# Optimization experiments

Hardware: AMD Instinct MI355X
Metric: run time of the kernel (lower is better)

## Reference

```python
import jax, jax.numpy as jnp
import numpy as np

POOL_SIZE = 7
NUM_ROIS = 1024
H, W, C = 256, 256, 512


def setup_inputs() -> dict:
    key = jax.random.key(0)
    k_img, k_xy, k_wh = jax.random.split(key, 3)
    img = jax.random.normal(k_img, (1, H, W, C), dtype=jnp.float32)
    # Valid ROIs: top-left in [0, 192), size in [8, 64), clipped to image bounds.
    xy = jax.random.randint(k_xy, (1, NUM_ROIS, 2), 0, 192)          # (x1, y1)
    wh = jax.random.randint(k_wh, (1, NUM_ROIS, 2), 8, 64)           # (w, h)
    x1y1 = xy
    x2y2 = jnp.minimum(xy + wh, jnp.array([W, H]))
    rois = jnp.concatenate([x1y1, x2y2], axis=-1).astype(jnp.int32)  # [1, R, 4] = (x1, y1, x2, y2)
    return {"img": img, "rois": rois}


def _roi_resize(feat, roi, P):
    """Bilinear-resize crop feat[y1:y2, x1:x2, :] to (P, P) — TF1 legacy mapping.
    feat: [H, W, C] float, roi: [4] int32 (x1, y1, x2, y2). Returns [P, P, C]."""
    x1, y1, x2, y2 = roi[0], roi[1], roi[2], roi[3]
    h = (y2 - y1).astype(jnp.float32)
    w = (x2 - x1).astype(jnp.float32)
    # src coordinate (crop-relative) = out_idx * (in_size / out_size)
    ys = jnp.arange(P, dtype=jnp.float32) * (h / P)   # [P]
    xs = jnp.arange(P, dtype=jnp.float32) * (w / P)   # [P]
    y0 = jnp.floor(ys).astype(jnp.int32)
    x0 = jnp.floor(xs).astype(jnp.int32)
    y1i = jnp.minimum(y0 + 1, jnp.maximum(y2 - y1 - 1, 0))
    x1i = jnp.minimum(x0 + 1, jnp.maximum(x2 - x1 - 1, 0))
    wy = (ys - y0.astype(jnp.float32))[:, None, None]  # [P,1,1]
    wx = (xs - x0.astype(jnp.float32))[None, :, None]  # [1,P,1]
    r0, r1 = y1 + y0, y1 + y1i                         # absolute rows
    c0, c1 = x1 + x0, x1 + x1i                         # absolute cols
    v00 = feat[r0[:, None], c0[None, :], :]            # [P,P,C]
    v01 = feat[r0[:, None], c1[None, :], :]
    v10 = feat[r1[:, None], c0[None, :], :]
    v11 = feat[r1[:, None], c1[None, :], :]
    return (v00 * (1.0 - wy) * (1.0 - wx) + v01 * (1.0 - wy) * wx
            + v10 * wy * (1.0 - wx) + v11 * wy * wx)


def reference(img, rois):
    feat = img[0]                                       # [H, W, C]
    pooled = jax.vmap(_roi_resize, in_axes=(None, 0, None))(feat, rois[0], POOL_SIZE)
    return pooled[None]                                 # [1, num_rois, P, P, C]
```

## Files before the change

### kernel.cpp

```cpp
#include <hip/hip_runtime.h>

#define POOL 7
#define IMG_W 256
#define IMG_C 512
#define NUM_ROIS 1024

typedef float f4 __attribute__((ext_vector_type(4)));

__global__ __launch_bounds__(128) void roi_pool_kernel(
    const float* __restrict__ img,
    const int*   __restrict__ rois,
    float*       __restrict__ out)
{
    const int bid  = blockIdx.x;
    const int xcd  = bid & 7;
    const int slot = bid >> 3;
    const int rloc = slot / POOL;
    const int py   = slot - rloc * POOL;
    const int roi  = xcd * (NUM_ROIS / 8) + rloc;

    const int4 rb = ((const int4*)rois)[roi];
    const int x1 = __builtin_amdgcn_readfirstlane(rb.x);
    const int y1 = __builtin_amdgcn_readfirstlane(rb.y);
    const int x2 = __builtin_amdgcn_readfirstlane(rb.z);
    const int y2 = __builtin_amdgcn_readfirstlane(rb.w);

    const float h = (float)(y2 - y1);
    const float w = (float)(x2 - x1);
    const float sy = h / (float)POOL;
    const float sx = w / (float)POOL;

    const float ys = (float)py * sy;
    const int   y0 = (int)floorf(ys);
    const int   y1i = min(y0 + 1, max(y2 - y1 - 1, 0));
    const float wy = ys - (float)y0;

    const size_t rowstride = (size_t)IMG_W * IMG_C;
    const float* row0 = img + (size_t)(y1 + y0)  * rowstride;
    const float* row1 = img + (size_t)(y1 + y1i) * rowstride;

    const int t = threadIdx.x;
    f4* obase = (f4*)out + ((size_t)roi * (POOL * POOL) + (size_t)py * POOL) * (IMG_C / 4) + t;

    const int cmax = max(x2 - x1 - 1, 0);

#pragma unroll
    for (int px = 0; px < POOL; ++px) {
        const float xs = (float)px * sx;
        const int   x0 = (int)floorf(xs);
        const int   x1i = min(x0 + 1, cmax);
        const float wx = xs - (float)x0;
        const int c0 = x1 + x0, c1 = x1 + x1i;

        const f4 v00 = ((const f4*)(row0 + (size_t)c0 * IMG_C))[t];
        const f4 v01 = ((const f4*)(row0 + (size_t)c1 * IMG_C))[t];
        const f4 v10 = ((const f4*)(row1 + (size_t)c0 * IMG_C))[t];
        const f4 v11 = ((const f4*)(row1 + (size_t)c1 * IMG_C))[t];

        const float w00 = (1.0f - wy) * (1.0f - wx);
        const float w01 = (1.0f - wy) * wx;
        const float w10 = wy * (1.0f - wx);
        const float w11 = wy * wx;

        f4 o = v00 * w00 + v01 * w01 + v10 * w10 + v11 * w11;
        __builtin_nontemporal_store(o, obase + px * (IMG_C / 4));
    }
}

extern "C" void kernel_launch(void* const* d_in, const int* in_sizes, int n_in,
                              void* d_out, int out_size, void* d_ws, size_t ws_size,
                              hipStream_t stream) {
    const float* img  = (const float*)d_in[0];
    const int*   rois = (const int*)d_in[1];
    float* out = (float*)d_out;

    dim3 grid(NUM_ROIS * POOL);
    dim3 block(128);
    roi_pool_kernel<<<grid, block, 0, stream>>>(img, rois, out);
}
```

Baseline: 236.5 us.

## Sort ROIs by spatial bin so blocks on an XCD share cached image rows

Adds a one-block counting-sort kernel that orders ROIs by a coarse 32x32-pixel spatial bucket of their top-left corner. The pooling kernel then processes ROIs in this sorted order, so ROIs handled by the same XCD are spatially close and reuse image data in that XCD's L2. The cost is an extra kernel launch, a dependent index load per block, and workspace use, and output writes become scattered across ROIs.

Result: no change. 234.9 us (-0.7%).

```diff
diff --git a/kernel.cpp b/kernel.cpp
--- a/kernel.cpp
+++ b/kernel.cpp
@@ -7,17 +7,45 @@
 
 typedef float f4 __attribute__((ext_vector_type(4)));
 
+__global__ __launch_bounds__(1024) void sort_rois_kernel(
+    const int* __restrict__ rois, int* __restrict__ order)
+{
+    __shared__ int hist[64];
+    __shared__ int base[64];
+    const int tid = threadIdx.x;
+
+    if (tid < 64) hist[tid] = 0;
+    __syncthreads();
+
+    const int x1 = rois[4 * tid + 0];
+    const int y1 = rois[4 * tid + 1];
+    const int key = ((y1 >> 5) << 3) | (x1 >> 5);
+    const int rank = atomicAdd(&hist[key], 1);
+    __syncthreads();
+
+    if (tid == 0) {
+        int run = 0;
+#pragma unroll
+        for (int k = 0; k < 64; ++k) { base[k] = run; run += hist[k]; }
+    }
+    __syncthreads();
+
+    order[base[key] + rank] = tid;
+}
+
 __global__ __launch_bounds__(128) void roi_pool_kernel(
     const float* __restrict__ img,
     const int*   __restrict__ rois,
+    const int*   __restrict__ order,
     float*       __restrict__ out)
 {
     const int bid  = blockIdx.x;
     const int xcd  = bid & 7;
     const int slot = bid >> 3;
-    const int rloc = slot / POOL;
-    const int py   = slot - rloc * POOL;
-    const int roi  = xcd * (NUM_ROIS / 8) + rloc;
+    const int sloc = slot / POOL;
+    const int py   = slot - sloc * POOL;
+    const int sidx = xcd * (NUM_ROIS / 8) + sloc;
+    const int roi  = order[sidx];
 
     const int4 rb = ((const int4*)rois)[roi];
     const int x1 = __builtin_amdgcn_readfirstlane(rb.x);
@@ -40,9 +68,9 @@
     const float* row1 = img + (size_t)(y1 + y1i) * rowstride;
 
     const int t = threadIdx.x;
+    const int cmax = max(x2 - x1 - 1, 0);
+
     f4* obase = (f4*)out + ((size_t)roi * (POOL * POOL) + (size_t)py * POOL) * (IMG_C / 4) + t;
-
-    const int cmax = max(x2 - x1 - 1, 0);
 
 #pragma unroll
     for (int px = 0; px < POOL; ++px) {
@@ -73,8 +101,8 @@
     const float* img  = (const float*)d_in[0];
     const int*   rois = (const int*)d_in[1];
     float* out = (float*)d_out;
+    int* order = (int*)d_ws;
 
-    dim3 grid(NUM_ROIS * POOL);
-    dim3 block(128);
-    roi_pool_kernel<<<grid, block, 0, stream>>>(img, rois, out);
+    sort_rois_kernel<<<1, 1024, 0, stream>>>(rois, order);
+    roi_pool_kernel<<<NUM_ROIS * POOL, 128, 0, stream>>>(img, rois, order, out);
 }
```
